# Optimization experiments

Measured on AMD Instinct MI355X. Metric: run time of the kernel, lower is better.

Reference implementation:

```python
import jax, jax.numpy as jnp
import numpy as np

NF = 64        # num_feat
B = 4
H = 128
W = 128
KH = KW = 3
K = KH * KW    # 9 kernel taps
DG = 1         # deformable_groups


def conv3x3(x, w, b):
    y = jax.lax.conv_general_dilated(
        x, w, window_strides=(1, 1), padding=((1, 1), (1, 1)),
        dimension_numbers=('NCHW', 'OIHW', 'NCHW'))
    return y + b[None, :, None, None]


def lrelu(x):
    return jnp.where(x >= 0, x, 0.1 * x)


def modulated_deform_conv(x, offset, mask, w, b):
    """DCNv2: bilinear gather at learned offsets, modulated by sigmoid mask.
    x: [B,C,H,W], offset: [B,2K,H,W] (y,x interleaved per tap), mask: [B,K,H,W].
    stride=1, padding=1, dilation=1, zero outside boundaries (mmcv semantics).
    """
    Bb, C, Hh, Ww = x.shape
    off = offset.reshape(Bb, K, 2, Hh, Ww)
    oy, ox = off[:, :, 0], off[:, :, 1]
    ki = (jnp.arange(K) // KW - 1).astype(x.dtype)  # dilation*i - pad
    kj = (jnp.arange(K) % KW - 1).astype(x.dtype)
    py = jnp.arange(Hh, dtype=x.dtype)[None, None, :, None] + ki[None, :, None, None] + oy  # [B,K,H,W]
    px = jnp.arange(Ww, dtype=x.dtype)[None, None, None, :] + kj[None, :, None, None] + ox
    y0 = jnp.floor(py)
    x0 = jnp.floor(px)
    wy1 = py - y0
    wx1 = px - x0
    x_flat = x.reshape(Bb, C, Hh * Ww)

    def gather(yi, xi):
        valid = (yi >= 0) & (yi < Hh) & (xi >= 0) & (xi < Ww)
        yc = jnp.clip(yi, 0, Hh - 1).astype(jnp.int32)
        xc = jnp.clip(xi, 0, Ww - 1).astype(jnp.int32)
        idx = (yc * Ww + xc).reshape(Bb, -1)                      # [B, K*H*W]
        g = jax.vmap(lambda xf, i: jnp.take(xf, i, axis=1))(x_flat, idx)  # [B,C,K*H*W]
        g = g.reshape(Bb, C, K, Hh, Ww)
        return g * valid[:, None].astype(x.dtype)

    v00 = gather(y0, x0)
    v01 = gather(y0, x0 + 1)
    v10 = gather(y0 + 1, x0)
    v11 = gather(y0 + 1, x0 + 1)
    wy = wy1[:, None]
    wx = wx1[:, None]
    samp = (v00 * (1 - wy) * (1 - wx) + v01 * (1 - wy) * wx
            + v10 * wy * (1 - wx) + v11 * wy * wx)                # [B,C,K,H,W]
    samp = samp * mask[:, None]
    out = jnp.einsum('bckhw,ock->bohw', samp, w.reshape(w.shape[0], C, K))
    return out + b[None, :, None, None]


def setup_inputs() -> dict:
    key = jax.random.key(0)
    ks = jax.random.split(key, 12)
    s = 0.05
    return {
        'nbr_feat_l': jax.random.normal(ks[0], (B, NF, H, W), jnp.float32),
        'ref_feat_l': jax.random.normal(ks[1], (B, NF, H, W), jnp.float32),
        'w1': jax.random.normal(ks[2], (NF, 2 * NF, 3, 3), jnp.float32) * s,
        'b1': jnp.zeros((NF,), jnp.float32),
        'w2': jax.random.normal(ks[3], (NF, NF, 3, 3), jnp.float32) * s,
        'b2': jnp.zeros((NF,), jnp.float32),
        'w3': jax.random.normal(ks[4], (NF, NF, 3, 3), jnp.float32) * s,
        'b3': jnp.zeros((NF,), jnp.float32),
        'w_off': jax.random.normal(ks[5], (DG * 3 * K, NF, 3, 3), jnp.float32) * s,
        'b_off': jnp.zeros((DG * 3 * K,), jnp.float32),
        'w_dcn': jax.random.normal(ks[6], (NF, NF, 3, 3), jnp.float32) * s,
        'b_dcn': jnp.zeros((NF,), jnp.float32),
    }


def reference(nbr_feat_l, ref_feat_l, w1, b1, w2, b2, w3, b3, w_off, b_off, w_dcn, b_dcn):
    o = jnp.concatenate([nbr_feat_l, ref_feat_l], axis=1)
    o = lrelu(conv3x3(o, w1, b1))
    o = lrelu(conv3x3(o, w2, b2))
    o = lrelu(conv3x3(o, w3, b3))
    out = conv3x3(o, w_off, b_off)                      # [B, 27, H, W]
    o1, o2, m = jnp.split(out, 3, axis=1)
    offset = 15 * jnp.tanh(jnp.concatenate([o1, o2], axis=1))  # [B, 18, H, W]
    mask = jax.nn.sigmoid(m)                                   # [B, 9, H, W]
    feat = lrelu(modulated_deform_conv(nbr_feat_l, offset, mask, w_dcn, b_dcn))
    return feat, offset, mask
```

## Files before the change

kernel.cpp:

```cpp
#include <hip/hip_runtime.h>
#include <math.h>


typedef _Float16 h8 __attribute__((ext_vector_type(8)));
typedef _Float16 h4 __attribute__((ext_vector_type(4)));
typedef _Float16 h2 __attribute__((ext_vector_type(2)));
typedef float f4 __attribute__((ext_vector_type(4)));

__global__ __launch_bounds__(256) void setup_kernel(
    const float* __restrict__ nbr, const float* __restrict__ refp,
    const float* __restrict__ w1, const float* __restrict__ w2,
    const float* __restrict__ w3, const float* __restrict__ w_off,
    const float* __restrict__ w_dcn,
    _Float16* __restrict__ X1, _Float16* __restrict__ X2,
    _Float16* __restrict__ B64, _Float16* __restrict__ C64,
    _Float16* __restrict__ wF1, _Float16* __restrict__ wF2,
    _Float16* __restrict__ wF3, _Float16* __restrict__ wFo,
    _Float16* __restrict__ wFd) {
  __shared__ float t[64 * 65];
  int bid = blockIdx.x;
  int tid = threadIdx.x;
  if (bid < 792) {
    int i = bid * 256 + tid;
    if (i < 73728) {
      int j = i;
      int icw = j & 31; int t1 = j >> 5; int oc = t1 & 63; int t2 = t1 >> 6;
      int ch = t2 & 3; int tap = t2 >> 2; int ic = ch * 32 + icw;
      wF1[j] = (_Float16)w1[(oc * 128 + ic) * 9 + tap];
    } else if (i < 110592) {
      int j = i - 73728;
      int icw = j & 31; int t1 = j >> 5; int oc = t1 & 63; int t2 = t1 >> 6;
      int ch = t2 & 1; int tap = t2 >> 1; int ic = ch * 32 + icw;
      wF2[j] = (_Float16)w2[(oc * 64 + ic) * 9 + tap];
    } else if (i < 147456) {
      int j = i - 110592;
      int icw = j & 31; int t1 = j >> 5; int oc = t1 & 63; int t2 = t1 >> 6;
      int ch = t2 & 1; int tap = t2 >> 1; int ic = ch * 32 + icw;
      wF3[j] = (_Float16)w3[(oc * 64 + ic) * 9 + tap];
    } else if (i < 165888) {
      int jj = i - 147456;
      int pc = jj >> 10;
      int mt = (jj >> 9) & 1;
      int Lx = (jj >> 3) & 63;
      int e  = jj & 7;
      int tap = pc >> 1, c = pc & 1;
      int oc = mt * 16 + (Lx & 15);
      int ic = c * 32 + (Lx >> 4) * 8 + e;
      float v = (oc < 27) ? w_off[(oc * 64 + ic) * 9 + tap] : 0.f;
      wFo[jj] = (_Float16)v;
    } else if (i < 202752) {
      int jj = i - 165888;
      int ks = jj >> 11;
      int mt = (jj >> 9) & 3;
      int Lx = (jj >> 3) & 63;
      int e  = jj & 7;
      int k = ks >> 1, s = ks & 1;
      int oc = mt * 16 + (Lx & 15);
      int ch = s * 32 + (Lx >> 4) * 8 + e;
      wFd[jj] = (_Float16)w_dcn[(oc * 64 + ch) * 9 + k];
    }
    return;
  }
  if (bid < 1050) {
    int i = (bid - 792) * 256 + tid;
    int bufi = i / 16512;
    int j = i - bufi * 16512;
    int b = j / 4128;
    int r = j - b * 4128;
    int p = r >> 3; int cg = r & 7;
    int row, col;
    if (p < 130)      { row = 0;   col = p; }
    else if (p < 260) { row = 129; col = p - 130; }
    else if (p < 388) { row = 1 + (p - 260); col = 0; }
    else              { row = 1 + (p - 388); col = 129; }
    _Float16* dst = (bufi == 0) ? X1 : (bufi == 1) ? X2 : (bufi == 2) ? B64 : C64;
    uint4 z; z.x = z.y = z.z = z.w = 0u;
    *(uint4*)(dst + ((size_t)(b * 130 + row) * 130 + col) * 64 + cg * 8) = z;
    return;
  }
  int j = bid - 1050;
  int half = j & 1;
  int y = (j >> 1) & 127;
  int b = (j >> 8) & 3;
  int src = j >> 10;
  const float* sp = src ? refp : nbr;
  _Float16* dst = src ? X2 : X1;
  for (int l = tid; l < 64 * 64; l += 256) {
    int c = l >> 6, gx = l & 63;
    t[c * 65 + gx] = sp[(((size_t)b * 64 + c) << 14) + (y << 7) + half * 64 + gx];
  }
  __syncthreads();
  unsigned* dstU = (unsigned*)dst;
  for (int l = tid; l < 64 * 32; l += 256) {
    int pxl = l >> 5, c2 = l & 31;
    union { _Float16 h[2]; unsigned u; } pk;
    pk.h[0] = (_Float16)t[(2 * c2) * 65 + pxl];
    pk.h[1] = (_Float16)t[(2 * c2 + 1) * 65 + pxl];
    dstU[((size_t)(b * 130 + y + 1) * 130 + 1 + half * 64 + pxl) * 32 + c2] = pk.u;
  }
}

template <int NCH, bool SPLIT>
__global__ __launch_bounds__(256, 2) void conv3x3_ks_kernel(
    const _Float16* __restrict__ X1, const _Float16* __restrict__ X2,
    const _Float16* __restrict__ W, const float* __restrict__ bias,
    _Float16* __restrict__ outP) {
  __shared__ f4 Lred[2][16][64];
  int tid = threadIdx.x;
  int wv = tid >> 6, L = tid & 63;
  int lm = L & 15, lq = L >> 4;
  int pr = wv >> 1;
  int kw = wv & 1;
  int bid = blockIdx.x;
  int xcd = bid & 7, j = bid >> 3;
  int y = (xcd << 4) | (j & 15);
  int b = j >> 4;
  int px0 = pr * 64;

  f4 acc[4][4];
#pragma unroll
  for (int i = 0; i < 4; ++i)
#pragma unroll
    for (int n = 0; n < 4; ++n) acc[i][n] = (f4)0.f;

#pragma unroll
  for (int ci = 0; ci < NCH / 2; ++ci) {
    int c = kw * (NCH / 2) + ci;
    const _Float16* src = (SPLIT && c >= 2) ? X2 : X1;
    int cl = SPLIT ? (c & 1) : c;
#pragma unroll
    for (int tap = 0; tap < 9; ++tap) {
      const int dy = tap / 3 - 1, dx = tap % 3 - 1;
      const _Float16* xb = src + ((size_t)((b * 130 + (y + 1 + dy)) * 130) + (1 + dx) + px0) * 64
                               + cl * 32 + lq * 8;
      h8 b0 = *(const h8*)(xb + lm * 64);
      h8 b1 = *(const h8*)(xb + (16 + lm) * 64);
      h8 b2 = *(const h8*)(xb + (32 + lm) * 64);
      h8 b3 = *(const h8*)(xb + (48 + lm) * 64);
      const _Float16* wp = W + (size_t)((tap * NCH + c) * 64) * 32 + lm * 32 + lq * 8;
      h8 a0 = *(const h8*)(wp);
      h8 a1 = *(const h8*)(wp + 512);
      h8 a2 = *(const h8*)(wp + 1024);
      h8 a3 = *(const h8*)(wp + 1536);
#pragma unroll
      for (int mt = 0; mt < 4; ++mt) {
        h8 am = (mt == 0) ? a0 : (mt == 1) ? a1 : (mt == 2) ? a2 : a3;
        acc[mt][0] = __builtin_amdgcn_mfma_f32_16x16x32_f16(am, b0, acc[mt][0], 0, 0, 0);
        acc[mt][1] = __builtin_amdgcn_mfma_f32_16x16x32_f16(am, b1, acc[mt][1], 0, 0, 0);
        acc[mt][2] = __builtin_amdgcn_mfma_f32_16x16x32_f16(am, b2, acc[mt][2], 0, 0, 0);
        acc[mt][3] = __builtin_amdgcn_mfma_f32_16x16x32_f16(am, b3, acc[mt][3], 0, 0, 0);
      }
    }
  }
  if (kw) {
#pragma unroll
    for (int mt = 0; mt < 4; ++mt)
#pragma unroll
      for (int nt = 0; nt < 4; ++nt)
        Lred[pr][mt * 4 + nt][L] = acc[mt][nt];
  }
  __syncthreads();
  if (kw == 0) {
#pragma unroll
    for (int mt = 0; mt < 4; ++mt)
#pragma unroll
      for (int nt = 0; nt < 4; ++nt)
        acc[mt][nt] += Lred[pr][mt * 4 + nt][L];
    const size_t obase = ((size_t)(b * 130 + (y + 1)) * 130 + 1) * 64;
#pragma unroll
    for (int mt = 0; mt < 4; ++mt)
#pragma unroll
      for (int nt = 0; nt < 4; ++nt) {
        int px = px0 + nt * 16 + lm;
        h4 pk;
#pragma unroll
        for (int r = 0; r < 4; ++r) {
          int oc = mt * 16 + lq * 4 + r;
          float v = acc[mt][nt][r] + bias[oc];
          v = (v >= 0.f) ? v : 0.1f * v;
          pk[r] = (_Float16)v;
        }
        *(h4*)(outP + obase + (size_t)px * 64 + mt * 16 + lq * 4) = pk;
      }
  }
}

__global__ __launch_bounds__(256, 4) void off_dcn_kernel(
    const _Float16* __restrict__ Xc, const _Float16* __restrict__ Xs,
    const _Float16* __restrict__ Wo, const float* __restrict__ bo,
    const _Float16* __restrict__ wD, const float* __restrict__ bd,
    float* __restrict__ off_out, float* __restrict__ mask_out,
    float* __restrict__ out) {
  __shared__ float Soff[4][16][28];
  int tid = threadIdx.x;
  int wv = tid >> 6, L = tid & 63;
  int lm = L & 15, lq = L >> 4;
  int lq8 = lq * 8;
  int g = blockIdx.x;
  int xcd = g & 7;
  int r0 = g >> 3;
  int half = r0 & 1;
  int y = (xcd << 4) | ((r0 >> 1) & 15);
  int b = r0 >> 5;
  int px0 = half * 64 + wv * 16;
  int gpx = px0 + lm;
  int hw = (y << 7) + gpx;
  int rb = b * 130;

  {
    f4 oa[2];
    oa[0] = (f4)0.f; oa[1] = (f4)0.f;
#pragma unroll
    for (int c = 0; c < 2; ++c)
#pragma unroll
      for (int tap = 0; tap < 9; ++tap) {
        const int dy = tap / 3 - 1, dx = tap % 3 - 1;
        const _Float16* xb = Xc + ((size_t)((rb + (y + 1 + dy)) * 130) + (1 + dx) + px0) * 64
                                + c * 32 + lq8;
        h8 b0 = *(const h8*)(xb + lm * 64);
        const _Float16* wp = Wo + (size_t)(tap * 2 + c) * 1024 + L * 8;
        h8 a0 = *(const h8*)(wp);
        h8 a1 = *(const h8*)(wp + 512);
        oa[0] = __builtin_amdgcn_mfma_f32_16x16x32_f16(a0, b0, oa[0], 0, 0, 0);
        oa[1] = __builtin_amdgcn_mfma_f32_16x16x32_f16(a1, b0, oa[1], 0, 0, 0);
      }
#pragma unroll
    for (int mt = 0; mt < 2; ++mt)
#pragma unroll
      for (int r = 0; r < 4; ++r) {
        int oc = mt * 16 + lq * 4 + r;
        if (oc < 18) {
          float v = 15.f * tanhf(oa[mt][r] + bo[oc]);
          off_out[((b * 18 + oc) << 14) + hw] = v;
          Soff[wv][lm][oc] = v;
        } else if (oc < 27) {
          float v = 1.f / (1.f + expf(-(oa[mt][r] + bo[oc])));
          mask_out[((b * 9 + (oc - 18)) << 14) + hw] = v;
          Soff[wv][lm][oc] = v;
        }
      }
  }

  f4 acc[4];
#pragma unroll
  for (int mm = 0; mm < 4; ++mm) acc[mm] = (f4)0.f;

  const char* Xb = (const char*)Xs;
  const int cbL = lq8 * 2;

#pragma unroll
  for (int gp = 0; gp < 3; ++gp) {
    float soy[3], sox[3], som[3];
#pragma unroll
    for (int t = 0; t < 3; ++t) {
      const int k = gp * 3 + t;
      soy[t] = Soff[wv][lm][2 * k];
      sox[t] = Soff[wv][lm][2 * k + 1];
      som[t] = Soff[wv][lm][18 + k];
    }
    int ro0[3], ro1[3], co0[3], co1[3];
    h2 Wc00[3], Wc01[3], Wc10[3], Wc11[3];
#pragma unroll
    for (int t = 0; t < 3; ++t) {
      const int k = gp * 3 + t;
      const int kr = k / 3, kc = k - kr * 3;
      float py = (float)(y + kr - 1) + soy[t];
      float pxf = (float)(gpx + kc - 1) + sox[t];
      float fy = floorf(py), fx = floorf(pxf);
      float wy = py - fy, wx = pxf - fx;
      int y0 = (int)fy, x0 = (int)fx;
      int y1 = y0 + 1, x1 = x0 + 1;
      float vy0 = ((unsigned)y0 < 128u) ? 1.f : 0.f;
      float vy1 = ((unsigned)y1 < 128u) ? 1.f : 0.f;
      float vx0 = ((unsigned)x0 < 128u) ? 1.f : 0.f;
      float vx1 = ((unsigned)x1 < 128u) ? 1.f : 0.f;
      float ey = 1.f - wy, ex = 1.f - wx;
      float mk = som[t];
      _Float16 w00 = (_Float16)(ey * ex * mk * vy0 * vx0);
      _Float16 w01 = (_Float16)(ey * wx * mk * vy0 * vx1);
      _Float16 w10 = (_Float16)(wy * ex * mk * vy1 * vx0);
      _Float16 w11 = (_Float16)(wy * wx * mk * vy1 * vx1);
      Wc00[t] = (h2){w00, w00}; Wc01[t] = (h2){w01, w01};
      Wc10[t] = (h2){w10, w10}; Wc11[t] = (h2){w11, w11};
      int y0c = min(max(y0, 0), 127) + 1, y1c = min(max(y1, 0), 127) + 1;
      int x0c = min(max(x0, 0), 127) + 1, x1c = min(max(x1, 0), 127) + 1;
      ro0[t] = (rb + y0c) * 16640;
      ro1[t] = (rb + y1c) * 16640;
      co0[t] = x0c * 128;
      co1[t] = x1c * 128;
    }
#pragma unroll
    for (int s = 0; s < 2; ++s) {
      const int cb2 = cbL + s * 64;
      h8 gv[12];
#pragma unroll
      for (int t = 0; t < 3; ++t) {
        gv[t * 4 + 0] = *(const h8*)(Xb + (ro0[t] + co0[t] + cb2));
        gv[t * 4 + 1] = *(const h8*)(Xb + (ro0[t] + co1[t] + cb2));
        gv[t * 4 + 2] = *(const h8*)(Xb + (ro1[t] + co0[t] + cb2));
        gv[t * 4 + 3] = *(const h8*)(Xb + (ro1[t] + co1[t] + cb2));
      }
#pragma unroll
      for (int t = 0; t < 3; ++t) {
        const int k = gp * 3 + t;
        h8 bv;
#pragma unroll
        for (int j2 = 0; j2 < 4; ++j2) {
          h2 a  = {gv[t * 4 + 0][2 * j2], gv[t * 4 + 0][2 * j2 + 1]};
          h2 bb = {gv[t * 4 + 1][2 * j2], gv[t * 4 + 1][2 * j2 + 1]};
          h2 cc = {gv[t * 4 + 2][2 * j2], gv[t * 4 + 2][2 * j2 + 1]};
          h2 dd = {gv[t * 4 + 3][2 * j2], gv[t * 4 + 3][2 * j2 + 1]};
          h2 r = a * Wc00[t];
          r += bb * Wc01[t];
          r += cc * Wc10[t];
          r += dd * Wc11[t];
          bv[2 * j2] = r[0];
          bv[2 * j2 + 1] = r[1];
        }
        const _Float16* wp = wD + (size_t)(k * 2 + s) * 2048 + L * 8;
        acc[0] = __builtin_amdgcn_mfma_f32_16x16x32_f16(*(const h8*)(wp), bv, acc[0], 0, 0, 0);
        acc[1] = __builtin_amdgcn_mfma_f32_16x16x32_f16(*(const h8*)(wp + 512), bv, acc[1], 0, 0, 0);
        acc[2] = __builtin_amdgcn_mfma_f32_16x16x32_f16(*(const h8*)(wp + 1024), bv, acc[2], 0, 0, 0);
        acc[3] = __builtin_amdgcn_mfma_f32_16x16x32_f16(*(const h8*)(wp + 1536), bv, acc[3], 0, 0, 0);
      }
    }
  }

#pragma unroll
  for (int mt = 0; mt < 4; ++mt)
#pragma unroll
    for (int r = 0; r < 4; ++r) {
      int oc = mt * 16 + lq * 4 + r;
      float v = acc[mt][r] + bd[oc];
      v = (v >= 0.f) ? v : 0.1f * v;
      out[(((b << 6) + oc) << 14) + (y << 7) + gpx] = v;
    }
}

extern "C" void kernel_launch(void* const* d_in, const int* in_sizes, int n_in,
                              void* d_out, int out_size, void* d_ws, size_t ws_size,
                              hipStream_t stream) {
  const float* nbr   = (const float*)d_in[0];
  const float* refp  = (const float*)d_in[1];
  const float* w1    = (const float*)d_in[2];
  const float* b1    = (const float*)d_in[3];
  const float* w2    = (const float*)d_in[4];
  const float* b2    = (const float*)d_in[5];
  const float* w3    = (const float*)d_in[6];
  const float* b3    = (const float*)d_in[7];
  const float* w_off = (const float*)d_in[8];
  const float* b_off = (const float*)d_in[9];
  const float* w_dcn = (const float*)d_in[10];
  const float* b_dcn = (const float*)d_in[11];

  float* outp = (float*)d_out;
  float* feat = outp;
  float* offp = outp + 4194304;
  float* mskp = outp + 4194304 + 1179648;

  char* ws = (char*)d_ws;
  const size_t PB = 8652800;
  _Float16* X1  = (_Float16*)ws;
  _Float16* X2  = (_Float16*)(ws + PB);
  _Float16* B64 = (_Float16*)(ws + 2 * PB);
  _Float16* C64 = (_Float16*)(ws + 3 * PB);
  char* p = ws + 4 * PB;
  _Float16* wF1 = (_Float16*)p;  p += (size_t)73728 * 2;
  _Float16* wF2 = (_Float16*)p;  p += (size_t)36864 * 2;
  _Float16* wF3 = (_Float16*)p;  p += (size_t)36864 * 2;
  _Float16* wFo = (_Float16*)p;  p += (size_t)18432 * 2;
  _Float16* wFd = (_Float16*)p;

  setup_kernel<<<dim3(3098), 256, 0, stream>>>(nbr, refp, w1, w2, w3, w_off, w_dcn,
                                               X1, X2, B64, C64, wF1, wF2, wF3, wFo, wFd);
  conv3x3_ks_kernel<4, true><<<dim3(512), 256, 0, stream>>>(X1, X2, wF1, b1, B64);
  conv3x3_ks_kernel<2, false><<<dim3(512), 256, 0, stream>>>(B64, nullptr, wF2, b2, C64);
  conv3x3_ks_kernel<2, false><<<dim3(512), 256, 0, stream>>>(C64, nullptr, wF3, b3, B64);
  off_dcn_kernel<<<dim3(1024), 256, 0, stream>>>(B64, X1, wFo, b_off, wFd, b_dcn,
                                                 offp, mskp, feat);
}
```

Baseline: 229.1 us.

## Stage conv input rows into LDS via async loads and split output channels across waves

The three 3x3 conv kernels now copy the three padded input rows for a 64-pixel half-row into shared memory with global_load_lds, using an XOR swizzle to avoid bank conflicts. All nine taps then read B fragments from LDS instead of issuing repeated global loads. Work is split by output channels across two waves rather than by input-channel halves, which removes the LDS reduction step. The grid doubles to 1024 blocks of 128 threads. The costs are an added barrier and serialized staging (two stages for the split first layer), with no overlap of loads and compute.

```diff
diff --git a/kernel.cpp b/kernel.cpp
--- a/kernel.cpp
+++ b/kernel.cpp
@@ -101,88 +101,107 @@
 }
 
 template <int NCH, bool SPLIT>
-__global__ __launch_bounds__(256, 2) void conv3x3_ks_kernel(
+__global__ __launch_bounds__(128, 4) void conv3x3_lds_kernel(
     const _Float16* __restrict__ X1, const _Float16* __restrict__ X2,
     const _Float16* __restrict__ W, const float* __restrict__ bias,
     _Float16* __restrict__ outP) {
-  __shared__ f4 Lred[2][16][64];
+  __shared__ _Float16 Lb[3 * 72 * 64];
   int tid = threadIdx.x;
   int wv = tid >> 6, L = tid & 63;
   int lm = L & 15, lq = L >> 4;
-  int pr = wv >> 1;
-  int kw = wv & 1;
   int bid = blockIdx.x;
   int xcd = bid & 7, j = bid >> 3;
-  int y = (xcd << 4) | (j & 15);
-  int b = j >> 4;
-  int px0 = pr * 64;
-
-  f4 acc[4][4];
-#pragma unroll
-  for (int i = 0; i < 4; ++i)
-#pragma unroll
-    for (int n = 0; n < 4; ++n) acc[i][n] = (f4)0.f;
-
-#pragma unroll
-  for (int ci = 0; ci < NCH / 2; ++ci) {
-    int c = kw * (NCH / 2) + ci;
-    const _Float16* src = (SPLIT && c >= 2) ? X2 : X1;
-    int cl = SPLIT ? (c & 1) : c;
-#pragma unroll
-    for (int tap = 0; tap < 9; ++tap) {
-      const int dy = tap / 3 - 1, dx = tap % 3 - 1;
-      const _Float16* xb = src + ((size_t)((b * 130 + (y + 1 + dy)) * 130) + (1 + dx) + px0) * 64
-                               + cl * 32 + lq * 8;
-      h8 b0 = *(const h8*)(xb + lm * 64);
-      h8 b1 = *(const h8*)(xb + (16 + lm) * 64);
-      h8 b2 = *(const h8*)(xb + (32 + lm) * 64);
-      h8 b3 = *(const h8*)(xb + (48 + lm) * 64);
-      const _Float16* wp = W + (size_t)((tap * NCH + c) * 64) * 32 + lm * 32 + lq * 8;
-      h8 a0 = *(const h8*)(wp);
-      h8 a1 = *(const h8*)(wp + 512);
-      h8 a2 = *(const h8*)(wp + 1024);
-      h8 a3 = *(const h8*)(wp + 1536);
-#pragma unroll
-      for (int mt = 0; mt < 4; ++mt) {
-        h8 am = (mt == 0) ? a0 : (mt == 1) ? a1 : (mt == 2) ? a2 : a3;
-        acc[mt][0] = __builtin_amdgcn_mfma_f32_16x16x32_f16(am, b0, acc[mt][0], 0, 0, 0);
-        acc[mt][1] = __builtin_amdgcn_mfma_f32_16x16x32_f16(am, b1, acc[mt][1], 0, 0, 0);
-        acc[mt][2] = __builtin_amdgcn_mfma_f32_16x16x32_f16(am, b2, acc[mt][2], 0, 0, 0);
-        acc[mt][3] = __builtin_amdgcn_mfma_f32_16x16x32_f16(am, b3, acc[mt][3], 0, 0, 0);
-      }
-    }
-  }
-  if (kw) {
-#pragma unroll
-    for (int mt = 0; mt < 4; ++mt)
-#pragma unroll
-      for (int nt = 0; nt < 4; ++nt)
-        Lred[pr][mt * 4 + nt][L] = acc[mt][nt];
-  }
+  int half = j & 1;
+  int y = (xcd << 4) | ((j >> 1) & 15);
+  int b = j >> 5;
+  int px0 = half * 64;
+
+  auto stage = [&](const _Float16* Xsrc) {
+    const char* Xb = (const char*)Xsrc;
+    size_t rb0 = ((size_t)(b * 130 + y) * 130 + px0) * 128;
+    for (int i = wv; i < 27; i += 2) {
+      int o = i * 1024 + L * 16;
+      int row = o / 9216;
+      int orow = o - row * 9216;
+      int px = orow >> 7;
+      int c2 = (orow >> 4) & 7;
+      size_t src = rb0 + (size_t)row * 16640 + (size_t)(px << 7) + (((c2 ^ (px & 7))) << 4);
+      __builtin_amdgcn_global_load_lds(
+          (const __attribute__((address_space(1))) void*)(Xb + src),
+          (__attribute__((address_space(3))) void*)((char*)Lb + i * 1024), 16, 0, 0);
+    }
+  };
+
+  f4 acc[2][4];
+#pragma unroll
+  for (int m = 0; m < 2; ++m)
+#pragma unroll
+    for (int n = 0; n < 4; ++n) acc[m][n] = (f4)0.f;
+
+  auto compute = [&](int cbase) {
+#pragma unroll
+    for (int ci = 0; ci < 2; ++ci) {
+      int c = cbase + ci;
+#pragma unroll
+      for (int tg = 0; tg < 3; ++tg) {
+        h8 a[6];
+#pragma unroll
+        for (int t = 0; t < 3; ++t) {
+          int tap = tg * 3 + t;
+          const _Float16* wp = W + (size_t)((tap * NCH + c) * 64 + wv * 32 + lm) * 32 + lq * 8;
+          a[2 * t]     = *(const h8*)(wp);
+          a[2 * t + 1] = *(const h8*)(wp + 512);
+        }
+#pragma unroll
+        for (int t = 0; t < 3; ++t) {
+          int tap = tg * 3 + t;
+          const int dy = tap / 3, dx = tap % 3;
+          h8 bf[4];
+#pragma unroll
+          for (int g = 0; g < 4; ++g) {
+            int pxcol = g * 16 + lm + dx;
+            int chunk = (ci * 4 + lq) ^ (pxcol & 7);
+            int off = dy * 9216 + (pxcol << 7) + (chunk << 4);
+            bf[g] = *(const h8*)((const char*)Lb + off);
+          }
+#pragma unroll
+          for (int g = 0; g < 4; ++g) {
+            acc[0][g] = __builtin_amdgcn_mfma_f32_16x16x32_f16(a[2 * t], bf[g], acc[0][g], 0, 0, 0);
+            acc[1][g] = __builtin_amdgcn_mfma_f32_16x16x32_f16(a[2 * t + 1], bf[g], acc[1][g], 0, 0, 0);
+          }
+        }
+      }
+    }
+  };
+
+  stage(SPLIT ? X1 : X1);
+  asm volatile("s_waitcnt vmcnt(0)" ::: "memory");
   __syncthreads();
-  if (kw == 0) {
-#pragma unroll
-    for (int mt = 0; mt < 4; ++mt)
-#pragma unroll
-      for (int nt = 0; nt < 4; ++nt)
-        acc[mt][nt] += Lred[pr][mt * 4 + nt][L];
-    const size_t obase = ((size_t)(b * 130 + (y + 1)) * 130 + 1) * 64;
-#pragma unroll
-    for (int mt = 0; mt < 4; ++mt)
-#pragma unroll
-      for (int nt = 0; nt < 4; ++nt) {
-        int px = px0 + nt * 16 + lm;
-        h4 pk;
-#pragma unroll
-        for (int r = 0; r < 4; ++r) {
-          int oc = mt * 16 + lq * 4 + r;
-          float v = acc[mt][nt][r] + bias[oc];
-          v = (v >= 0.f) ? v : 0.1f * v;
-          pk[r] = (_Float16)v;
-        }
-        *(h4*)(outP + obase + (size_t)px * 64 + mt * 16 + lq * 4) = pk;
-      }
-  }
+  compute(0);
+  if (SPLIT) {
+    __syncthreads();
+    stage(X2);
+    asm volatile("s_waitcnt vmcnt(0)" ::: "memory");
+    __syncthreads();
+    compute(2);
+  }
+
+  const size_t obase = ((size_t)(b * 130 + (y + 1)) * 130 + 1 + px0) * 64;
+#pragma unroll
+  for (int mt = 0; mt < 2; ++mt)
+#pragma unroll
+    for (int nt = 0; nt < 4; ++nt) {
+      int px = nt * 16 + lm;
+      h4 pk;
+#pragma unroll
+      for (int r = 0; r < 4; ++r) {
+        int oc = wv * 32 + mt * 16 + lq * 4 + r;
+        float v = acc[mt][nt][r] + bias[oc];
+        v = (v >= 0.f) ? v : 0.1f * v;
+        pk[r] = (_Float16)v;
+      }
+      *(h4*)(outP + obase + (size_t)px * 64 + wv * 32 + mt * 16 + lq * 4) = pk;
+    }
 }
 
 __global__ __launch_bounds__(256, 4) void off_dcn_kernel(
@@ -373,9 +392,9 @@
 
   setup_kernel<<<dim3(3098), 256, 0, stream>>>(nbr, refp, w1, w2, w3, w_off, w_dcn,
                                                X1, X2, B64, C64, wF1, wF2, wF3, wFo, wFd);
-  conv3x3_ks_kernel<4, true><<<dim3(512), 256, 0, stream>>>(X1, X2, wF1, b1, B64);
-  conv3x3_ks_kernel<2, false><<<dim3(512), 256, 0, stream>>>(B64, nullptr, wF2, b2, C64);
-  conv3x3_ks_kernel<2, false><<<dim3(512), 256, 0, stream>>>(C64, nullptr, wF3, b3, B64);
+  conv3x3_lds_kernel<4, true><<<dim3(1024), 128, 0, stream>>>(X1, X2, wF1, b1, B64);
+  conv3x3_lds_kernel<2, false><<<dim3(1024), 128, 0, stream>>>(B64, nullptr, wF2, b2, C64);
+  conv3x3_lds_kernel<2, false><<<dim3(1024), 128, 0, stream>>>(C64, nullptr, wF3, b3, B64);
   off_dcn_kernel<<<dim3(1024), 256, 0, stream>>>(B64, X1, wFo, b_off, wFd, b_dcn,
                                                  offp, mskp, feat);
 }
```

After: 203.2 us. 1.13x faster.
